# Kernel optimization log

Measured on AMD Instinct MI355X. Metric: run time of the kernel, lower is better.

The kernel has to match this reference:

```python
import jax, jax.numpy as jnp
import numpy as np

THRESHOLD = 1.0
DECAY = 0.95
T, B, N_IN = 16, 512, 3072
S1, S2, S3 = 256, 256, 128
E = 8


def _lif_step(v, h):
    # LIF membrane update: decay, integrate, threshold-spike, soft reset.
    v = v * DECAY + h
    spk = (v >= THRESHOLD).astype(v.dtype)
    return spk, v - spk * THRESHOLD


def setup_inputs() -> dict:
    key = jax.random.key(0)
    k_seq, k1, k2, k3 = jax.random.split(key, 4)
    # Binary spike train input (rate-coded), shape (T, B, N_in)
    spike_seq = (jax.random.uniform(k_seq, (T, B, N_IN)) < 0.5).astype(jnp.float32)
    # Expert weights: nn.Linear weight layout is (out, in); init N(0, 0.05)
    W1 = 0.05 * jax.random.normal(k1, (E, S1, N_IN), dtype=jnp.float32)
    W2 = 0.05 * jax.random.normal(k2, (E, S2, S1), dtype=jnp.float32)
    W3 = 0.05 * jax.random.normal(k3, (E, S3, S2), dtype=jnp.float32)
    # Uniform gates 1/num_experts (requires_grad=False buffers in the original)
    g = jnp.full((E,), 1.0 / E, dtype=jnp.float32)
    return {"spike_seq": spike_seq, "W1": W1, "W2": W2, "W3": W3,
            "g1": g, "g2": g, "g3": g}


def reference(spike_seq, W1, W2, W3, g1, g2, g3):
    t, b = spike_seq.shape[0], spike_seq.shape[1]
    x = spike_seq.reshape(t, b, -1)
    e = W1.shape[0]
    dt = x.dtype
    v1 = jnp.zeros((e, b, W1.shape[1]), dt)
    v2 = jnp.zeros((e, b, W2.shape[1]), dt)
    v3 = jnp.zeros((e, b, W3.shape[1]), dt)

    def step(carry, xt):
        v1, v2, v3 = carry
        # stage 1: batched per-expert GEMM + LIF + gated combine
        h1 = jnp.einsum('bi,eoi->ebo', xt, W1)
        spk1, v1 = _lif_step(v1, h1)
        c1 = jnp.einsum('e,ebo->bo', g1, spk1)
        # stage 2
        h2 = jnp.einsum('bi,eoi->ebo', c1, W2)
        spk2, v2 = _lif_step(v2, h2)
        c2 = jnp.einsum('e,ebo->bo', g2, spk2)
        # stage 3
        h3 = jnp.einsum('bi,eoi->ebo', c2, W3)
        spk3, v3 = _lif_step(v3, h3)
        c3 = jnp.einsum('e,ebo->bo', g3, spk3)
        return (v1, v2, v3), (c1, c2, c3)

    _, (s1, s2, s3) = jax.lax.scan(step, (v1, v2, v3), x)
    # time-averaged combined outputs per stage
    return s1.mean(axis=0), s2.mean(axis=0), s3.mean(axis=0)
```

## Files before the change

kernel.cpp:

```cpp
#include <hip/hip_runtime.h>
#include <hip/hip_bf16.h>
#include <cmath>

#define T_STEPS 16
#define BATCH   512
#define N_IN    3072
#define S1      256
#define S2      256
#define S3      128
#define NEXP    8
#define M_ROWS  (T_STEPS * BATCH)
#define MT_ALL  (M_ROWS / 32)

typedef int v4i  __attribute__((ext_vector_type(4)));
typedef int v16i __attribute__((ext_vector_type(16)));
typedef unsigned long long u64;
typedef unsigned int uint32;

__device__ __forceinline__ v4i unpack16_bits(uint32 w16)
{
    v4i d;
    #pragma unroll
    for (int c = 0; c < 4; ++c) {
        uint32 x = (w16 >> (4 * c)) & 0xFu;
        x = x + (x << 7);
        x = x + (x << 14);
        d[c] = (int)(x & 0x01010101u);
    }
    return d;
}

template<int S, int K>
__device__ __forceinline__ void digitize_chunk(
    const float* __restrict__ W, char* __restrict__ Bf, int t)
{
    int lane16 = t & 63;
    int o  = (t >> 6) & (S - 1);
    int kb = t >> ((S == 256) ? 14 : 13);
    int r  = lane16 & 31;
    int qd = lane16 >> 5;
    int e    = r >> 2;
    int limb = r & 3;
    int k0 = kb * 32 + qd * 16;

    const float4* Wp = (const float4*)(W + ((size_t)e * S + o) * K + k0);
    char out[16];
    #pragma unroll
    for (int f4 = 0; f4 < 4; ++f4) {
        float4 w = Wp[f4];
        float ws[4] = {w.x, w.y, w.z, w.w};
        #pragma unroll
        for (int c = 0; c < 4; ++c) {
            long long q = llrint((double)ws[c] * 4294967296.0);
            int d = 0;
            #pragma unroll
            for (int l = 0; l < 4; ++l) {
                int dl = (int)((q + 128) & 255) - 128;
                q = (q - dl) >> 8;
                if (l == limb) d = dl;
            }
            out[f4 * 4 + c] = (char)d;
        }
    }
    *(v4i*)(Bf + (size_t)t * 16) = *(v4i*)out;
}

__global__ __launch_bounds__(256) void prep(
    const float* __restrict__ x,  const float* __restrict__ W1,
    const float* __restrict__ W2, const float* __restrict__ W3,
    u64* __restrict__ bitsT, char* __restrict__ B1f,
    char* __restrict__ B2f,  char* __restrict__ B3f)
{
    const int bid = blockIdx.x;
    const int tid = threadIdx.x;
    if (bid < 98304) {
        int gid = bid * 256 + tid;
        float v = x[gid];
        u64 m = __ballot(v >= 0.5f);
        if ((tid & 63) == 0) {
            int tb = gid / N_IN;
            int k  = gid - tb * N_IN;
            int t  = tb >> 9;
            int b  = tb & 511;
            bitsT[(size_t)(k >> 6) * M_ROWS + (b * 16 + t)] = m;
        }
    } else if (bid < 98304 + 4608) {
        int t    = (bid - 98304) * 256 + tid;
        int l16  = t & 63;
        int tt   = t >> 6;
        int tile = tt % 192;
        int kb   = tt / 192;
        int gr   = tile * 32 + (l16 & 31);
        int qd   = l16 >> 5;
        int o    = gr / 24;
        int rem  = gr - o * 24;
        int e    = rem / 3;
        int limb = rem - e * 3;
        int k0   = kb * 32 + qd * 16;
        const float4* Wp = (const float4*)(W1 + ((size_t)e * S1 + o) * N_IN + k0);
        char out[16];
        #pragma unroll
        for (int f4 = 0; f4 < 4; ++f4) {
            float4 w = Wp[f4];
            float ws[4] = {w.x, w.y, w.z, w.w};
            #pragma unroll
            for (int c = 0; c < 4; ++c) {
                long long q = llrint((double)ws[c] * 16777216.0);
                int d0 = (int)((q + 128) & 255) - 128;
                long long q1 = (q - d0) >> 8;
                int d1 = (int)((q1 + 128) & 255) - 128;
                int d2 = (int)((q1 - d1) >> 8);
                int d  = (limb == 0) ? d0 : ((limb == 1) ? d1 : d2);
                out[f4 * 4 + c] = (char)d;
            }
        }
        *(v4i*)(B1f + (size_t)t * 16) = *(v4i*)out;
    } else if (bid < 98304 + 4608 + 512) {
        digitize_chunk<S2, S1>(W2, B2f, (bid - 98304 - 4608) * 256 + tid);
    } else {
        digitize_chunk<S3, S2>(W3, B3f, (bid - 98304 - 4608 - 512) * 256 + tid);
    }
}

__global__ __launch_bounds__(256, 3) void fused_stage1(
    const u64* __restrict__ AT0, const char* __restrict__ Bf,
    const float* __restrict__ g, char* __restrict__ Cf,
    float* __restrict__ Mean)
{
    constexpr int KI    = N_IN / 64;
    constexpr int NTILES = 192;
    constexpr int BSTEP = 2 * NTILES * 1024;
    constexpr int KSOFF = NTILES * 1024;
    __shared__ long long hsI[128 * 32];

    const int tid  = threadIdx.x;
    const int lane = tid & 63;
    const int w    = tid >> 6;
    const int col  = lane & 31;
    const int qd   = lane >> 5;
    const int wm   = w * 32;

    #pragma unroll
    for (int i = 0; i < 16; ++i) hsI[tid + i * 256] = 0;
    __syncthreads();

    const int id    = blockIdx.x;
    const int xcd   = id & 7;
    const int inner = id >> 3;
    const int nblk  = xcd * 8 + (inner >> 6);
    const int mblk  = inner & 63;
    const int m0    = mblk * 128;

    const u64* AT = AT0 + (m0 + wm + col);
    const int sh16 = qd * 16;
    const char* Bu = Bf + (size_t)nblk * 3 * 1024 + lane * 16;

    v16i acc[3];
    #pragma unroll
    for (int j = 0; j < 3; ++j)
        #pragma unroll
        for (int r = 0; r < 16; ++r) acc[j][r] = 0;

    u64 ab[3];
    v4i Bb[3][6];

    #pragma unroll
    for (int s = 0; s < 2; ++s) {
        ab[s] = AT[(size_t)s * M_ROWS];
        const char* bu = Bu + (size_t)s * BSTEP;
        #pragma unroll
        for (int ks = 0; ks < 2; ++ks)
            #pragma unroll
            for (int jj = 0; jj < 3; ++jj)
                Bb[s][ks * 3 + jj] = *(const v4i*)(bu + ks * KSOFF + jj * 1024);
    }

    auto body = [&](int it, int cur, int pf) {
        const int itp = it + 2;
        ab[pf] = AT[(size_t)itp * M_ROWS];
        const char* bu = Bu + (size_t)itp * BSTEP;
        #pragma unroll
        for (int ks = 0; ks < 2; ++ks)
            #pragma unroll
            for (int jj = 0; jj < 3; ++jj)
                Bb[pf][ks * 3 + jj] = *(const v4i*)(bu + ks * KSOFF + jj * 1024);
        __builtin_amdgcn_s_setprio(1);
        #pragma unroll
        for (int ks = 0; ks < 2; ++ks) {
            uint32 dw = ks ? (uint32)(ab[cur] >> 32) : (uint32)ab[cur];
            v4i af = unpack16_bits(dw >> sh16);
            #pragma unroll
            for (int jj = 0; jj < 3; ++jj)
                acc[jj] = __builtin_amdgcn_mfma_i32_32x32x32_i8(
                    af, Bb[cur][ks * 3 + jj], acc[jj], 0, 0, 0);
        }
        __builtin_amdgcn_s_setprio(0);
    };

    for (int it = 0; it < KI; it += 3) {
        __builtin_amdgcn_s_barrier();
        body(it + 0, 0, 2);
        body(it + 1, 1, 0);
        body(it + 2, 2, 1);
    }

    int ocol[3], lsh[3];
    #pragma unroll
    for (int jj = 0; jj < 3; ++jj) {
        int grb   = jj * 32 + col;
        int o_rel = grb / 24;
        int rem   = grb - o_rel * 24;
        int e_    = rem / 3;
        int limb  = rem - e_ * 3;
        ocol[jj]  = o_rel * 8 + e_;
        lsh[jj]   = limb * 8;
    }
    #pragma unroll
    for (int jj = 0; jj < 3; ++jj)
        #pragma unroll
        for (int reg = 0; reg < 16; ++reg) {
            int m = wm + (reg & 3) + 8 * (reg >> 2) + 4 * qd;
            atomicAdd((unsigned long long*)&hsI[m * 32 + ocol[jj]],
                      (unsigned long long)((long long)acc[jj][reg] << lsh[jj]));
        }
    __syncthreads();

    const int b_loc = tid >> 5;
    const int oe    = tid & 31;
    const int o_loc = oe >> 3;
    const int e     = tid & 7;
    const float ge  = g[e];
    const int bg = mblk * 8 + b_loc;
    const int og = nblk * 4 + o_loc;

    const int kb_a   = og >> 5;
    const int qd_a   = (og >> 4) & 1;
    const int byte_a = og & 15;

    const double sc = 1.0 / 16777216.0;
    double v = 0.0;
    float gacc = 0.0f;
    #pragma unroll
    for (int t = 0; t < T_STEPS; ++t) {
        double h  = (double)hsI[(b_loc * 16 + t) * 32 + oe] * sc;
        double vv = v * 0.95 + h;
        int spk = (vv >= 1.0) ? 1 : 0;
        v = vv - (double)spk;
        float gs = ge * (float)spk;
        gs += __shfl_xor(gs, 1);
        gs += __shfl_xor(gs, 2);
        gs += __shfl_xor(gs, 4);
        gacc += gs;
        int cnt = spk;
        cnt += __shfl_xor(cnt, 1);
        cnt += __shfl_xor(cnt, 2);
        cnt += __shfl_xor(cnt, 4);
        if (e == 0) {
            int mp = bg * 16 + t;
            int lane_a = (mp & 31) + 32 * qd_a;
            Cf[(((size_t)kb_a * MT_ALL + (mp >> 5)) * 64 + lane_a) * 16 + byte_a]
                = (char)cnt;
        }
    }
    if (e == 0) Mean[(size_t)bg * S1 + og] = gacc * 0.0625f;
}

template<int K, int S, int SHIFT, bool WRITEC, int NBLK, int MINW>
__global__ __launch_bounds__(256, MINW) void fused_stage(
    const char* __restrict__ Ap, const char* __restrict__ Bf,
    const float* __restrict__ g, char* __restrict__ Cf,
    float* __restrict__ Mean)
{
    constexpr int KI = K / 64;
    static_assert(KI % 2 == 0, "frag path wants even KI");
    constexpr int NT = S;
    constexpr int NS = NBLK / 8;
    __shared__ double hs[256][16];

    const int tid  = threadIdx.x;
    const int lane = tid & 63;
    const int w    = tid >> 6;
    const int col  = lane & 31;
    const int qd   = lane >> 5;
    const int wm   = w * 64;

    const int id    = blockIdx.x;
    const int xcd   = id & 7;
    const int inner = id >> 3;
    const int nblk  = xcd * NS + (inner >> 5);
    const int mblk  = inner & 31;
    const int m0    = mblk * 256;

    const int nt0 = nblk * 2;
    const char* Bbase = Bf + ((size_t)nt0 * 64 + lane) * 16;

    v16i acc[2][2];
    #pragma unroll
    for (int i = 0; i < 2; ++i)
        #pragma unroll
        for (int j = 0; j < 2; ++j)
            #pragma unroll
            for (int r = 0; r < 16; ++r) acc[i][j][r] = 0;

    auto loadB = [&](int kb, int jj) -> v4i {
        return *(const v4i*)(Bbase + (size_t)kb * (NT * 1024) + jj * 1024);
    };
    const int mt0 = (m0 + wm) >> 5;
    const char* Abase = Ap + ((size_t)mt0 * 64 + lane) * 16;
    auto loadA = [&](int kb, int ii) -> v4i {
        return *(const v4i*)(Abase + (size_t)kb * (MT_ALL * 1024) + ii * 1024);
    };

    v4i Ab[2][4];
    v4i Bb[2][4];

    #pragma unroll
    for (int ks = 0; ks < 2; ++ks) {
        Ab[0][ks * 2 + 0] = loadA(ks, 0);
        Ab[0][ks * 2 + 1] = loadA(ks, 1);
        #pragma unroll
        for (int jj = 0; jj < 2; ++jj)
            Bb[0][ks * 2 + jj] = loadB(ks, jj);
    }

    auto body = [&](int it, int cur, int pf) {
        const int itp = it + 1;
        #pragma unroll
        for (int ks = 0; ks < 2; ++ks) {
            Ab[pf][ks * 2 + 0] = loadA(itp * 2 + ks, 0);
            Ab[pf][ks * 2 + 1] = loadA(itp * 2 + ks, 1);
            #pragma unroll
            for (int jj = 0; jj < 2; ++jj)
                Bb[pf][ks * 2 + jj] = loadB(itp * 2 + ks, jj);
        }
        #pragma unroll
        for (int ks = 0; ks < 2; ++ks)
            #pragma unroll
            for (int jj = 0; jj < 2; ++jj) {
                acc[0][jj] = __builtin_amdgcn_mfma_i32_32x32x32_i8(Ab[cur][ks*2+0], Bb[cur][ks*2+jj], acc[0][jj], 0,0,0);
                acc[1][jj] = __builtin_amdgcn_mfma_i32_32x32x32_i8(Ab[cur][ks*2+1], Bb[cur][ks*2+jj], acc[1][jj], 0,0,0);
            }
    };
    for (int it = 0; it < KI; it += 2) {
        body(it + 0, 0, 1);
        body(it + 1, 1, 0);
    }

    const double sbase = 1.0 / (double)(1ll << SHIFT);
    #pragma unroll
    for (int j = 0; j < 2; ++j) {
        const int oe = j * 8 + (col >> 2);
        #pragma unroll
        for (int i = 0; i < 2; ++i) {
            #pragma unroll
            for (int reg = 0; reg < 16; ++reg) {
                int a = acc[i][j][reg];
                int s01 = a + (__shfl_xor(a, 1) << 8);
                int s23 = __shfl_xor(s01, 2);
                double d = ((double)s01 + 65536.0 * (double)s23) * sbase;
                if ((col & 3) == 0) {
                    int m = wm + i * 32 + (reg & 3) + 8 * (reg >> 2) + 4 * qd;
                    hs[m][oe] = d;
                }
            }
        }
    }
    __syncthreads();

    const int b_loc  = tid >> 4;
    const int o_loc  = (tid >> 3) & 1;
    const int e      = tid & 7;
    const int oe     = o_loc * 8 + e;
    const float ge   = g[e];
    const int bg = mblk * 16 + b_loc;
    const int og = nblk * 2 + o_loc;

    const int kb_a   = og >> 5;
    const int qd_a   = (og >> 4) & 1;
    const int byte_a = og & 15;

    double v = 0.0;
    float gacc = 0.0f;
    #pragma unroll
    for (int t = 0; t < T_STEPS; ++t) {
        double h  = hs[b_loc * 16 + t][oe];
        double vv = v * 0.95 + h;
        int spk = (vv >= 1.0) ? 1 : 0;
        v = vv - (double)spk;
        float gs = ge * (float)spk;
        gs += __shfl_xor(gs, 1);
        gs += __shfl_xor(gs, 2);
        gs += __shfl_xor(gs, 4);
        gacc += gs;
        if (WRITEC) {
            int cnt = spk;
            cnt += __shfl_xor(cnt, 1);
            cnt += __shfl_xor(cnt, 2);
            cnt += __shfl_xor(cnt, 4);
            if (e == 0) {
                int mp = bg * 16 + t;
                int lane_a = (mp & 31) + 32 * qd_a;
                Cf[(((size_t)kb_a * MT_ALL + (mp >> 5)) * 64 + lane_a) * 16 + byte_a]
                    = (char)cnt;
            }
        }
    }
    if (e == 0) Mean[(size_t)bg * S + og] = gacc * 0.0625f;
}

extern "C" void kernel_launch(void* const* d_in, const int* in_sizes, int n_in,
                              void* d_out, int out_size, void* d_ws, size_t ws_size,
                              hipStream_t stream) {
    const float* x  = (const float*)d_in[0];
    const float* W1 = (const float*)d_in[1];
    const float* W2 = (const float*)d_in[2];
    const float* W3 = (const float*)d_in[3];
    const float* g1 = (const float*)d_in[4];
    const float* g2 = (const float*)d_in[5];
    const float* g3 = (const float*)d_in[6];
    float* out = (float*)d_out;

    char* ws = (char*)d_ws;
    u64*  AbitsT = (u64*)ws;
    char* B1f    = ws + 4194304ull;
    char* B2f    = ws + 25165824ull;
    char* B3f    = ws + 28311552ull;
    char* c1f    = ws + 30408704ull;
    char* c2f    = ws + 34603008ull;

    dim3 blk(256);

    prep<<<98304 + 4608 + 512 + 256, blk, 0, stream>>>(
        x, W1, W2, W3, AbitsT, B1f, B2f, B3f);

    fused_stage1<<<64 * 64, blk, 0, stream>>>(AbitsT, B1f, g1, c1f, out);

    fused_stage<S1, S2, 35, true,  128, 3><<<32 * 128, blk, 0, stream>>>(
        c1f, B2f, g2, c2f, out + BATCH * S1);
    fused_stage<S2, S3, 35, false, 64, 3><<<32 * 64, blk, 0, stream>>>(
        c2f, B3f, g3, nullptr, out + BATCH * (S1 + S2));
}
```

Before: 489.4 us.

## Reorder W1 digit limbs so each wave owns one column per limb, drop LDS atomics

```diff
diff --git a/kernel.cpp b/kernel.cpp
--- a/kernel.cpp
+++ b/kernel.cpp
@@ -92,10 +92,10 @@
         int kb   = tt / 192;
         int gr   = tile * 32 + (l16 & 31);
         int qd   = l16 >> 5;
-        int o    = gr / 24;
-        int rem  = gr - o * 24;
-        int e    = rem / 3;
-        int limb = rem - e * 3;
+        int limb = gr >> 11;
+        int oe   = gr & 2047;
+        int o    = oe >> 3;
+        int e    = oe & 7;
         int k0   = kb * 32 + qd * 16;
         const float4* Wp = (const float4*)(W1 + ((size_t)e * S1 + o) * N_IN + k0);
         char out[16];
@@ -122,16 +122,15 @@
     }
 }
 
-__global__ __launch_bounds__(256, 3) void fused_stage1(
+__global__ __launch_bounds__(256, 4) void fused_stage1(
     const u64* __restrict__ AT0, const char* __restrict__ Bf,
     const float* __restrict__ g, char* __restrict__ Cf,
     float* __restrict__ Mean)
 {
-    constexpr int KI    = N_IN / 64;
-    constexpr int NTILES = 192;
-    constexpr int BSTEP = 2 * NTILES * 1024;
-    constexpr int KSOFF = NTILES * 1024;
-    __shared__ long long hsI[128 * 32];
+    constexpr int KI      = N_IN / 64;
+    constexpr int KSTRIDE = 192 * 1024;
+    constexpr int BSTEP   = 2 * KSTRIDE;
+    __shared__ double hs[128 * 32];
 
     const int tid  = threadIdx.x;
     const int lane = tid & 63;
@@ -140,10 +139,6 @@
     const int qd   = lane >> 5;
     const int wm   = w * 32;
 
-    #pragma unroll
-    for (int i = 0; i < 16; ++i) hsI[tid + i * 256] = 0;
-    __syncthreads();
-
     const int id    = blockIdx.x;
     const int xcd   = id & 7;
     const int inner = id >> 3;
@@ -153,7 +148,7 @@
 
     const u64* AT = AT0 + (m0 + wm + col);
     const int sh16 = qd * 16;
-    const char* Bu = Bf + (size_t)nblk * 3 * 1024 + lane * 16;
+    const char* Bu = Bf + (size_t)nblk * 1024 + lane * 16;
 
     v16i acc[3];
     #pragma unroll
@@ -161,29 +156,27 @@
         #pragma unroll
         for (int r = 0; r < 16; ++r) acc[j][r] = 0;
 
-    u64 ab[3];
-    v4i Bb[3][6];
-
-    #pragma unroll
-    for (int s = 0; s < 2; ++s) {
-        ab[s] = AT[(size_t)s * M_ROWS];
-        const char* bu = Bu + (size_t)s * BSTEP;
-        #pragma unroll
-        for (int ks = 0; ks < 2; ++ks)
-            #pragma unroll
-            for (int jj = 0; jj < 3; ++jj)
-                Bb[s][ks * 3 + jj] = *(const v4i*)(bu + ks * KSOFF + jj * 1024);
-    }
+    u64 ab[2];
+    v4i Bb[2][6];
+
+    ab[0] = AT[0];
+    #pragma unroll
+    for (int ks = 0; ks < 2; ++ks)
+        #pragma unroll
+        for (int jj = 0; jj < 3; ++jj)
+            Bb[0][ks * 3 + jj] =
+                *(const v4i*)(Bu + ks * KSTRIDE + jj * 65536);
 
     auto body = [&](int it, int cur, int pf) {
-        const int itp = it + 2;
+        const int itp = it + 1;
         ab[pf] = AT[(size_t)itp * M_ROWS];
         const char* bu = Bu + (size_t)itp * BSTEP;
         #pragma unroll
         for (int ks = 0; ks < 2; ++ks)
             #pragma unroll
             for (int jj = 0; jj < 3; ++jj)
-                Bb[pf][ks * 3 + jj] = *(const v4i*)(bu + ks * KSOFF + jj * 1024);
+                Bb[pf][ks * 3 + jj] =
+                    *(const v4i*)(bu + ks * KSTRIDE + jj * 65536);
         __builtin_amdgcn_s_setprio(1);
         #pragma unroll
         for (int ks = 0; ks < 2; ++ks) {
@@ -197,32 +190,19 @@
         __builtin_amdgcn_s_setprio(0);
     };
 
-    for (int it = 0; it < KI; it += 3) {
-        __builtin_amdgcn_s_barrier();
-        body(it + 0, 0, 2);
+    for (int it = 0; it < KI; it += 2) {
+        body(it + 0, 0, 1);
         body(it + 1, 1, 0);
-        body(it + 2, 2, 1);
-    }
-
-    int ocol[3], lsh[3];
-    #pragma unroll
-    for (int jj = 0; jj < 3; ++jj) {
-        int grb   = jj * 32 + col;
-        int o_rel = grb / 24;
-        int rem   = grb - o_rel * 24;
-        int e_    = rem / 3;
-        int limb  = rem - e_ * 3;
-        ocol[jj]  = o_rel * 8 + e_;
-        lsh[jj]   = limb * 8;
-    }
-    #pragma unroll
-    for (int jj = 0; jj < 3; ++jj)
-        #pragma unroll
-        for (int reg = 0; reg < 16; ++reg) {
-            int m = wm + (reg & 3) + 8 * (reg >> 2) + 4 * qd;
-            atomicAdd((unsigned long long*)&hsI[m * 32 + ocol[jj]],
-                      (unsigned long long)((long long)acc[jj][reg] << lsh[jj]));
-        }
+    }
+
+    const double sc = 1.0 / 16777216.0;
+    #pragma unroll
+    for (int reg = 0; reg < 16; ++reg) {
+        int m  = wm + (reg & 3) + 8 * (reg >> 2) + 4 * qd;
+        int lo = acc[0][reg] + (acc[1][reg] << 8);
+        double d = ((double)lo + 65536.0 * (double)acc[2][reg]) * sc;
+        hs[m * 32 + col] = d;
+    }
     __syncthreads();
 
     const int b_loc = tid >> 5;
@@ -237,12 +217,11 @@
     const int qd_a   = (og >> 4) & 1;
     const int byte_a = og & 15;
 
-    const double sc = 1.0 / 16777216.0;
     double v = 0.0;
     float gacc = 0.0f;
     #pragma unroll
     for (int t = 0; t < T_STEPS; ++t) {
-        double h  = (double)hsI[(b_loc * 16 + t) * 32 + oe] * sc;
+        double h  = hs[(b_loc * 16 + t) * 32 + oe];
         double vv = v * 0.95 + h;
         int spk = (vv >= 1.0) ? 1 : 0;
         v = vv - (double)spk;
```

Measured after the change: 500.2 us. +2.2%, slower.
